# Performance work log

Measured on AMD Instinct MI355X. Metric: run time of the kernel, lower is better.

Reference implementation:

```python
import jax, jax.numpy as jnp
import numpy as np

H = 256
V_IN = 32000
V_OUT = 32000
T = 2048


def setup_inputs() -> dict:
    key = jax.random.key(0)
    ks = jax.random.split(key, 16)
    s = 1.0 / np.sqrt(H)
    inp = {
        "src": jax.random.randint(ks[0], (T, 1), 0, V_IN, dtype=jnp.int64 if jax.config.jax_enable_x64 else jnp.int32),
        "trg": jax.random.randint(ks[1], (T, 1), 0, V_OUT, dtype=jnp.int64 if jax.config.jax_enable_x64 else jnp.int32),
        "enc_emb": jax.random.normal(ks[2], (V_IN, H), jnp.float32),
        "enc_W_ih": jax.random.uniform(ks[3], (3 * H, H), jnp.float32, -s, s),
        "enc_W_hh": jax.random.uniform(ks[4], (3 * H, H), jnp.float32, -s, s),
        "enc_b_ih": jax.random.uniform(ks[5], (3 * H,), jnp.float32, -s, s),
        "enc_b_hh": jax.random.uniform(ks[6], (3 * H,), jnp.float32, -s, s),
        "dec_emb": jax.random.normal(ks[7], (V_OUT, H), jnp.float32),
        "dec_W_ih": jax.random.uniform(ks[8], (3 * H, H), jnp.float32, -s, s),
        "dec_W_hh": jax.random.uniform(ks[9], (3 * H, H), jnp.float32, -s, s),
        "dec_b_ih": jax.random.uniform(ks[10], (3 * H,), jnp.float32, -s, s),
        "dec_b_hh": jax.random.uniform(ks[11], (3 * H,), jnp.float32, -s, s),
        "out_W": jax.random.uniform(ks[12], (V_OUT, H), jnp.float32, -s, s),
        "out_b": jax.random.uniform(ks[13], (V_OUT,), jnp.float32, -s, s),
    }
    return inp


def _gru_step(x, h, W_ih, W_hh, b_ih, b_hh):
    # PyTorch GRU cell math. x,h: [H]
    gi = W_ih @ x + b_ih          # [3H]
    gh = W_hh @ h + b_hh          # [3H]
    i_r, i_z, i_n = jnp.split(gi, 3)
    h_r, h_z, h_n = jnp.split(gh, 3)
    r = jax.nn.sigmoid(i_r + h_r)
    z = jax.nn.sigmoid(i_z + h_z)
    n = jnp.tanh(i_n + r * h_n)
    return (1.0 - z) * n + z * h


def reference(src, trg, enc_emb, enc_W_ih, enc_W_hh, enc_b_ih, enc_b_hh,
              dec_emb, dec_W_ih, dec_W_hh, dec_b_ih, dec_b_hh, out_W, out_b):
    src_t = src[:, 0]  # [T], batch forced to 1 by .view(1,1,-1)
    trg_t = trg[:, 0]  # [T]
    h0 = jnp.zeros((H,), enc_emb.dtype)

    def step(h, toks):
        s_tok, t_tok = toks
        # encoder step
        h = _gru_step(enc_emb[s_tok], h, enc_W_ih, enc_W_hh, enc_b_ih, enc_b_hh)
        # decoder step (relu on embedding per source)
        x_d = jax.nn.relu(dec_emb[t_tok])
        h = _gru_step(x_d, h, dec_W_ih, dec_W_hh, dec_b_ih, dec_b_hh)
        logits = out_W @ h + out_b          # [V_OUT]
        return h, jax.nn.log_softmax(logits)

    _, outs = jax.lax.scan(step, h0, (src_t, trg_t))
    return outs[:, None, :]  # [T, 1, V_OUT]
```

## Files before the change

### kernel.cpp

```cpp
#include <hip/hip_runtime.h>
#include <hip/hip_bf16.h>

#define T_STEPS 2048
#define HDIM 256
#define VOUT 32000

typedef short short8 __attribute__((ext_vector_type(8)));
typedef float f32x4 __attribute__((ext_vector_type(4)));

#if defined(__has_builtin)
#if __has_builtin(__builtin_amdgcn_sdot4)
#define HAVE_SDOT4 1
#endif
#if __has_builtin(__builtin_amdgcn_mov_dpp)
#define HAVE_DPP 1
#endif
#endif

__device__ __forceinline__ int dot4i8(int a, int b, int c) {
#ifdef HAVE_SDOT4
    return __builtin_amdgcn_sdot4(a, b, c, false);
#else
#pragma unroll
    for (int k = 0; k < 4; ++k) {
        int av = (a << (24 - 8 * k)) >> 24;
        int bv = (b << (24 - 8 * k)) >> 24;
        c += av * bv;
    }
    return c;
#endif
}

__device__ __forceinline__ int pairsum(int x) {
#ifdef HAVE_DPP
    return x + __builtin_amdgcn_mov_dpp(x, 0xB1, 0xF, 0xF, true);
#else
    return x + __shfl_xor(x, 1);
#endif
}

__device__ __forceinline__ float fast_sigmoid(float x) {
    return 1.0f / (1.0f + __expf(-x));
}
__device__ __forceinline__ float fast_tanh(float x) {
    float ax = fabsf(x);
    float e = __expf(-2.0f * ax);
    float t = 1.0f - 2.0f * e / (1.0f + e);
    return copysignf(t, x);
}

__global__ void k_quant(const float* __restrict__ W, int* __restrict__ wq,
                        float* __restrict__ sc) {
    int row = blockIdx.x;
    int t = threadIdx.x;
    float4 w = ((const float4*)(W + (size_t)row * HDIM))[t];
    float m = fmaxf(fmaxf(fabsf(w.x), fabsf(w.y)), fmaxf(fabsf(w.z), fabsf(w.w)));
#pragma unroll
    for (int off = 32; off; off >>= 1) m = fmaxf(m, __shfl_xor(m, off));
    float inv = (m > 0.0f) ? 127.0f / m : 0.0f;
    float scale = (m > 0.0f) ? m * (1.0f / 127.0f) : 0.0f;
    int q0 = __float2int_rn(w.x * inv); q0 = max(-127, min(127, q0));
    int q1 = __float2int_rn(w.y * inv); q1 = max(-127, min(127, q1));
    int q2 = __float2int_rn(w.z * inv); q2 = max(-127, min(127, q2));
    int q3 = __float2int_rn(w.w * inv); q3 = max(-127, min(127, q3));
    int packed = (q0 & 255) | ((q1 & 255) << 8) | ((q2 & 255) << 16) | ((q3 & 255) << 24);
    wq[row * 64 + t] = packed;
    if (t == 0) sc[row] = scale;
}

__global__ __launch_bounds__(256) void k_cvt(const float* __restrict__ in,
                                             unsigned short* __restrict__ out, int n4) {
    int i = blockIdx.x * 256 + threadIdx.x;
    if (i < n4) {
        float4 v = ((const float4*)in)[i];
        unsigned int u[4] = {__float_as_uint(v.x), __float_as_uint(v.y),
                             __float_as_uint(v.z), __float_as_uint(v.w)};
        ushort4 o;
        o.x = (unsigned short)((u[0] + 0x7FFFu + ((u[0] >> 16) & 1)) >> 16);
        o.y = (unsigned short)((u[1] + 0x7FFFu + ((u[1] >> 16) & 1)) >> 16);
        o.z = (unsigned short)((u[2] + 0x7FFFu + ((u[2] >> 16) & 1)) >> 16);
        o.w = (unsigned short)((u[3] + 0x7FFFu + ((u[3] >> 16) & 1)) >> 16);
        ((ushort4*)out)[i] = o;
    }
}

__global__ __launch_bounds__(256) void k_gi(const int* __restrict__ toks,
                                            const float* __restrict__ emb,
                                            const float* __restrict__ W,
                                            const float* __restrict__ b,
                                            float* __restrict__ gi, int do_relu) {
    __shared__ float4 xs[64];
    int t = blockIdx.x;
    int tid = threadIdx.x;
    int tok = toks[t];
    if (tid < 64) {
        float4 x = ((const float4*)(emb + (size_t)tok * HDIM))[tid];
        if (do_relu) {
            x.x = fmaxf(x.x, 0.0f); x.y = fmaxf(x.y, 0.0f);
            x.z = fmaxf(x.z, 0.0f); x.w = fmaxf(x.w, 0.0f);
        }
        xs[tid] = x;
    }
    __syncthreads();
#pragma unroll
    for (int g = 0; g < 3; ++g) {
        int row = tid + g * 256;
        const float4* wr = (const float4*)(W + (size_t)row * HDIM);
        float acc = b[row];
#pragma unroll 16
        for (int k = 0; k < 64; ++k) {
            float4 w = wr[k];
            float4 x = xs[k];
            acc += w.x * x.x + w.y * x.y + w.z * x.z + w.w * x.w;
        }
        gi[(size_t)t * 768 + row] = acc;
    }
}

__global__ __launch_bounds__(512, 2) void k_gru(
    const int* __restrict__ wq_e, const float* __restrict__ sc_e,
    const float* __restrict__ bhh_e, const float* __restrict__ gi_e,
    const int* __restrict__ wq_d, const float* __restrict__ sc_d,
    const float* __restrict__ bhh_d, const float* __restrict__ gi_d,
    unsigned short* __restrict__ h_bf) {
    __shared__ __align__(16) int HQ[2][64];

    const int tid = threadIdx.x;
    const int rg = tid >> 1;
    const int c  = tid & 1;

    int we[3][32], wd[3][32];
    float se[3], sd[3], be[3], bd[3];
#pragma unroll
    for (int j = 0; j < 3; ++j) {
        const int row = rg + j * 256;
        const int4* pe = (const int4*)(wq_e + (row * 64 + c * 32));
        const int4* pd = (const int4*)(wq_d + (row * 64 + c * 32));
#pragma unroll
        for (int i = 0; i < 8; ++i) {
            int4 a = pe[i];
            we[j][4 * i + 0] = a.x; we[j][4 * i + 1] = a.y;
            we[j][4 * i + 2] = a.z; we[j][4 * i + 3] = a.w;
            int4 bq = pd[i];
            wd[j][4 * i + 0] = bq.x; wd[j][4 * i + 1] = bq.y;
            wd[j][4 * i + 2] = bq.z; wd[j][4 * i + 3] = bq.w;
        }
        se[j] = sc_e[row] * (1.0f / 127.0f);
        sd[j] = sc_d[row] * (1.0f / 127.0f);
        be[j] = bhh_e[row];
        bd[j] = bhh_d[row];
    }

    float h = 0.0f;
    if (tid < 64) HQ[0][tid] = 0;
    __syncthreads();

    const float* ge = gi_e + rg;
    const float* gd = gi_d + rg;
    unsigned short* hop = h_bf + rg;
    int cur = 0;

    for (int t = 0; t < T_STEPS; ++t) {
        {
            float g0 = ge[0], g1 = ge[256], g2 = ge[512]; ge += 768;
            const int4* hq4 = ((const int4*)HQ[cur]) + c * 8;
            int p0 = 0, p1 = 0, p2 = 0;
#pragma unroll
            for (int i = 0; i < 8; ++i) {
                int4 v = hq4[i];
                p0 = dot4i8(we[0][4 * i + 0], v.x, p0);
                p1 = dot4i8(we[1][4 * i + 0], v.x, p1);
                p2 = dot4i8(we[2][4 * i + 0], v.x, p2);
                p0 = dot4i8(we[0][4 * i + 1], v.y, p0);
                p1 = dot4i8(we[1][4 * i + 1], v.y, p1);
                p2 = dot4i8(we[2][4 * i + 1], v.y, p2);
                p0 = dot4i8(we[0][4 * i + 2], v.z, p0);
                p1 = dot4i8(we[1][4 * i + 2], v.z, p1);
                p2 = dot4i8(we[2][4 * i + 2], v.z, p2);
                p0 = dot4i8(we[0][4 * i + 3], v.w, p0);
                p1 = dot4i8(we[1][4 * i + 3], v.w, p1);
                p2 = dot4i8(we[2][4 * i + 3], v.w, p2);
            }
            int f0 = pairsum(p0), f1 = pairsum(p1), f2 = pairsum(p2);
            float r = fast_sigmoid(g0 + se[0] * (float)f0 + be[0]);
            float z = fast_sigmoid(g1 + se[1] * (float)f1 + be[1]);
            float n = fast_tanh(g2 + r * (se[2] * (float)f2 + be[2]));
            h = (1.0f - z) * n + z * h;
            if (c == 0)
                ((signed char*)HQ[cur ^ 1])[rg] = (signed char)__float2int_rn(h * 127.0f);
        }
        __syncthreads();
        cur ^= 1;

        {
            float g0 = gd[0], g1 = gd[256], g2 = gd[512]; gd += 768;
            const int4* hq4 = ((const int4*)HQ[cur]) + c * 8;
            int p0 = 0, p1 = 0, p2 = 0;
#pragma unroll
            for (int i = 0; i < 8; ++i) {
                int4 v = hq4[i];
                p0 = dot4i8(wd[0][4 * i + 0], v.x, p0);
                p1 = dot4i8(wd[1][4 * i + 0], v.x, p1);
                p2 = dot4i8(wd[2][4 * i + 0], v.x, p2);
                p0 = dot4i8(wd[0][4 * i + 1], v.y, p0);
                p1 = dot4i8(wd[1][4 * i + 1], v.y, p1);
                p2 = dot4i8(wd[2][4 * i + 1], v.y, p2);
                p0 = dot4i8(wd[0][4 * i + 2], v.z, p0);
                p1 = dot4i8(wd[1][4 * i + 2], v.z, p1);
                p2 = dot4i8(wd[2][4 * i + 2], v.z, p2);
                p0 = dot4i8(wd[0][4 * i + 3], v.w, p0);
                p1 = dot4i8(wd[1][4 * i + 3], v.w, p1);
                p2 = dot4i8(wd[2][4 * i + 3], v.w, p2);
            }
            int f0 = pairsum(p0), f1 = pairsum(p1), f2 = pairsum(p2);
            float r = fast_sigmoid(g0 + sd[0] * (float)f0 + bd[0]);
            float z = fast_sigmoid(g1 + sd[1] * (float)f1 + bd[1]);
            float n = fast_tanh(g2 + r * (sd[2] * (float)f2 + bd[2]));
            h = (1.0f - z) * n + z * h;
            if (c == 0) {
                ((signed char*)HQ[cur ^ 1])[rg] = (signed char)__float2int_rn(h * 127.0f);
                unsigned int u = __float_as_uint(h);
                *hop = (unsigned short)((u + 0x7FFFu + ((u >> 16) & 1)) >> 16);
            }
            hop += 256;
        }
        __syncthreads();
        cur ^= 1;
    }
}

__global__ __launch_bounds__(256) void k_logits(const unsigned short* __restrict__ hb,
                                                const unsigned short* __restrict__ wb,
                                                const float* __restrict__ out_b,
                                                float* __restrict__ out) {
    const int vb = blockIdx.x * 64;
    const int tb = blockIdx.y * 64;
    const int w = threadIdx.x >> 6;
    const int l = threadIdx.x & 63;
    const int m = l & 15;
    const int q = l >> 4;

    const unsigned short* aptr = hb + (size_t)(tb + w * 16 + m) * HDIM + q * 8;
    const unsigned short* bptr = wb + (size_t)(vb + m) * HDIM + q * 8;

    short8 af[8];
#pragma unroll
    for (int kt = 0; kt < 8; ++kt) af[kt] = *(const short8*)(aptr + kt * 32);

    f32x4 acc[4];
#pragma unroll
    for (int nt = 0; nt < 4; ++nt)
#pragma unroll
        for (int r = 0; r < 4; ++r) acc[nt][r] = 0.0f;

#pragma unroll
    for (int nt = 0; nt < 4; ++nt) {
        const unsigned short* bp = bptr + (size_t)nt * 16 * HDIM;
#pragma unroll
        for (int kt = 0; kt < 8; ++kt) {
            short8 bf = *(const short8*)(bp + kt * 32);
            acc[nt] = __builtin_amdgcn_mfma_f32_16x16x32_bf16(af[kt], bf, acc[nt], 0, 0, 0);
        }
    }
#pragma unroll
    for (int nt = 0; nt < 4; ++nt) {
        float bias = out_b[vb + nt * 16 + m];
#pragma unroll
        for (int r = 0; r < 4; ++r) {
            out[(size_t)(tb + w * 16 + q * 4 + r) * VOUT + vb + nt * 16 + m] =
                acc[nt][r] + bias;
        }
    }
}

__global__ __launch_bounds__(256) void k_lse(const float* __restrict__ out,
                                             float* __restrict__ lse) {
    const int t = blockIdx.x;
    const int tid = threadIdx.x;
    const float* rowp = out + (size_t)t * VOUT;
    float m = -3.0e38f, l = 0.0f;
    for (int v = tid; v < VOUT; v += 256) {
        float x = rowp[v];
        float M = fmaxf(m, x);
        l = l * __expf(m - M) + __expf(x - M);
        m = M;
    }
#pragma unroll
    for (int off = 32; off; off >>= 1) {
        float m2 = __shfl_xor(m, off);
        float l2 = __shfl_xor(l, off);
        float M = fmaxf(m, m2);
        l = l * __expf(m - M) + l2 * __expf(m2 - M);
        m = M;
    }
    __shared__ float sm[4], sl[4];
    int lane = tid & 63, wv = tid >> 6;
    if (lane == 0) { sm[wv] = m; sl[wv] = l; }
    __syncthreads();
    if (tid == 0) {
        float M = fmaxf(fmaxf(sm[0], sm[1]), fmaxf(sm[2], sm[3]));
        float L = sl[0] * __expf(sm[0] - M) + sl[1] * __expf(sm[1] - M) +
                  sl[2] * __expf(sm[2] - M) + sl[3] * __expf(sm[3] - M);
        lse[t] = M + __logf(L);
    }
}

__global__ __launch_bounds__(256) void k_sub(float* __restrict__ out,
                                             const float* __restrict__ lse) {
    const int t = blockIdx.y;
    const int v4 = blockIdx.x * 256 + threadIdx.x;
    if (v4 < VOUT / 4) {
        float s = lse[t];
        float4* p = (float4*)(out + (size_t)t * VOUT) + v4;
        float4 o = *p;
        o.x -= s; o.y -= s; o.z -= s; o.w -= s;
        *p = o;
    }
}

extern "C" void kernel_launch(void* const* d_in, const int* in_sizes, int n_in,
                              void* d_out, int out_size, void* d_ws, size_t ws_size,
                              hipStream_t stream) {
    (void)in_sizes; (void)n_in; (void)out_size; (void)ws_size;
    const int*   src      = (const int*)d_in[0];
    const int*   trg      = (const int*)d_in[1];
    const float* enc_emb  = (const float*)d_in[2];
    const float* enc_W_ih = (const float*)d_in[3];
    const float* enc_W_hh = (const float*)d_in[4];
    const float* enc_b_ih = (const float*)d_in[5];
    const float* enc_b_hh = (const float*)d_in[6];
    const float* dec_emb  = (const float*)d_in[7];
    const float* dec_W_ih = (const float*)d_in[8];
    const float* dec_W_hh = (const float*)d_in[9];
    const float* dec_b_ih = (const float*)d_in[10];
    const float* dec_b_hh = (const float*)d_in[11];
    const float* out_W    = (const float*)d_in[12];
    const float* out_b    = (const float*)d_in[13];
    float* out = (float*)d_out;

    char* ws = (char*)d_ws;
    float* gi_e  = (float*)ws; ws += (size_t)T_STEPS * 768 * 4;
    float* gi_d  = (float*)ws; ws += (size_t)T_STEPS * 768 * 4;
    float* lse   = (float*)ws; ws += (size_t)T_STEPS * 4;
    float* sc_e  = (float*)ws; ws += 768 * 4;
    float* sc_d  = (float*)ws; ws += 768 * 4;
    int*   wq_e  = (int*)ws;   ws += 768 * 64 * 4;
    int*   wq_d  = (int*)ws;   ws += 768 * 64 * 4;
    unsigned short* h_bf = (unsigned short*)ws; ws += (size_t)T_STEPS * HDIM * 2;
    unsigned short* w_bf = (unsigned short*)ws; ws += (size_t)VOUT * HDIM * 2;

    k_quant<<<768, 64, 0, stream>>>(enc_W_hh, wq_e, sc_e);
    k_quant<<<768, 64, 0, stream>>>(dec_W_hh, wq_d, sc_d);
    k_cvt<<<(VOUT * HDIM / 4 + 255) / 256, 256, 0, stream>>>(out_W, w_bf, VOUT * HDIM / 4);
    k_gi<<<T_STEPS, 256, 0, stream>>>(src, enc_emb, enc_W_ih, enc_b_ih, gi_e, 0);
    k_gi<<<T_STEPS, 256, 0, stream>>>(trg, dec_emb, dec_W_ih, dec_b_ih, gi_d, 1);
    k_gru<<<1, 512, 0, stream>>>(wq_e, sc_e, enc_b_hh, gi_e,
                                 wq_d, sc_d, dec_b_hh, gi_d, h_bf);
    k_logits<<<dim3(VOUT / 64, T_STEPS / 64), 256, 0, stream>>>(h_bf, w_bf, out_b, out);
    k_lse<<<T_STEPS, 256, 0, stream>>>(out, lse);
    k_sub<<<dim3(32, T_STEPS), 256, 0, stream>>>(out, lse);
}
```

Measured before the change: 4.171 ms.

## Fuse log-sum-exp with subtraction, prefetch gate inputs, use rcp in GRU activations

Merges the lse and subtract kernels into one per-row kernel, so the separate launch and the lse buffer round trip go away. The row is read a second time, likely from cache. In the single-block GRU recurrence, the encoder and decoder input-gate values are now prefetched one phase early to hide global load latency on the serial critical path. The ping-pong index is replaced with two fixed shared buffers, and sigmoid and tanh now use hardware reciprocal instead of full division, which slightly changes numerics.

```diff
diff --git a/kernel.cpp b/kernel.cpp
--- a/kernel.cpp
+++ b/kernel.cpp
@@ -14,6 +14,9 @@
 #endif
 #if __has_builtin(__builtin_amdgcn_mov_dpp)
 #define HAVE_DPP 1
+#endif
+#if __has_builtin(__builtin_amdgcn_rcpf)
+#define HAVE_RCP 1
 #endif
 #endif
 
@@ -39,13 +42,21 @@
 #endif
 }
 
+__device__ __forceinline__ float fast_rcp(float x) {
+#ifdef HAVE_RCP
+    return __builtin_amdgcn_rcpf(x);
+#else
+    return 1.0f / x;
+#endif
+}
+
 __device__ __forceinline__ float fast_sigmoid(float x) {
-    return 1.0f / (1.0f + __expf(-x));
+    return fast_rcp(1.0f + __expf(-x));
 }
 __device__ __forceinline__ float fast_tanh(float x) {
     float ax = fabsf(x);
     float e = __expf(-2.0f * ax);
-    float t = 1.0f - 2.0f * e / (1.0f + e);
+    float t = 1.0f - 2.0f * e * fast_rcp(1.0f + e);
     return copysignf(t, x);
 }
 
@@ -123,7 +134,8 @@
     const int* __restrict__ wq_d, const float* __restrict__ sc_d,
     const float* __restrict__ bhh_d, const float* __restrict__ gi_d,
     unsigned short* __restrict__ h_bf) {
-    __shared__ __align__(16) int HQ[2][64];
+    __shared__ __align__(16) int HQA[64];
+    __shared__ __align__(16) int HQB[64];
 
     const int tid = threadIdx.x;
     const int rg = tid >> 1;
@@ -152,18 +164,21 @@
     }
 
     float h = 0.0f;
-    if (tid < 64) HQ[0][tid] = 0;
+    if (tid < 64) HQA[tid] = 0;
     __syncthreads();
 
     const float* ge = gi_e + rg;
     const float* gd = gi_d + rg;
     unsigned short* hop = h_bf + rg;
-    int cur = 0;
+
+    float eg0 = ge[0], eg1 = ge[256], eg2 = ge[512];
 
     for (int t = 0; t < T_STEPS; ++t) {
+        float dg0 = gd[0], dg1 = gd[256], dg2 = gd[512];
+        gd += 768;
+
         {
-            float g0 = ge[0], g1 = ge[256], g2 = ge[512]; ge += 768;
-            const int4* hq4 = ((const int4*)HQ[cur]) + c * 8;
+            const int4* hq4 = ((const int4*)HQA) + c * 8;
             int p0 = 0, p1 = 0, p2 = 0;
 #pragma unroll
             for (int i = 0; i < 8; ++i) {
@@ -182,19 +197,23 @@
                 p2 = dot4i8(we[2][4 * i + 3], v.w, p2);
             }
             int f0 = pairsum(p0), f1 = pairsum(p1), f2 = pairsum(p2);
-            float r = fast_sigmoid(g0 + se[0] * (float)f0 + be[0]);
-            float z = fast_sigmoid(g1 + se[1] * (float)f1 + be[1]);
-            float n = fast_tanh(g2 + r * (se[2] * (float)f2 + be[2]));
+            float r = fast_sigmoid(eg0 + se[0] * (float)f0 + be[0]);
+            float z = fast_sigmoid(eg1 + se[1] * (float)f1 + be[1]);
+            float n = fast_tanh(eg2 + r * (se[2] * (float)f2 + be[2]));
             h = (1.0f - z) * n + z * h;
             if (c == 0)
-                ((signed char*)HQ[cur ^ 1])[rg] = (signed char)__float2int_rn(h * 127.0f);
+                ((signed char*)HQB)[rg] = (signed char)__float2int_rn(h * 127.0f);
         }
         __syncthreads();
-        cur ^= 1;
 
         {
-            float g0 = gd[0], g1 = gd[256], g2 = gd[512]; gd += 768;
-            const int4* hq4 = ((const int4*)HQ[cur]) + c * 8;
+            const float* gen = (t < T_STEPS - 1) ? (ge + 768) : (gi_e + rg);
+            eg0 = gen[0]; eg1 = gen[256]; eg2 = gen[512];
+            ge = gen;
+        }
+
+        {
+            const int4* hq4 = ((const int4*)HQB) + c * 8;
             int p0 = 0, p1 = 0, p2 = 0;
 #pragma unroll
             for (int i = 0; i < 8; ++i) {
@@ -213,19 +232,18 @@
                 p2 = dot4i8(wd[2][4 * i + 3], v.w, p2);
             }
             int f0 = pairsum(p0), f1 = pairsum(p1), f2 = pairsum(p2);
-            float r = fast_sigmoid(g0 + sd[0] * (float)f0 + bd[0]);
-            float z = fast_sigmoid(g1 + sd[1] * (float)f1 + bd[1]);
-            float n = fast_tanh(g2 + r * (sd[2] * (float)f2 + bd[2]));
+            float r = fast_sigmoid(dg0 + sd[0] * (float)f0 + bd[0]);
+            float z = fast_sigmoid(dg1 + sd[1] * (float)f1 + bd[1]);
+            float n = fast_tanh(dg2 + r * (sd[2] * (float)f2 + bd[2]));
             h = (1.0f - z) * n + z * h;
             if (c == 0) {
-                ((signed char*)HQ[cur ^ 1])[rg] = (signed char)__float2int_rn(h * 127.0f);
+                ((signed char*)HQA)[rg] = (signed char)__float2int_rn(h * 127.0f);
                 unsigned int u = __float_as_uint(h);
                 *hop = (unsigned short)((u + 0x7FFFu + ((u >> 16) & 1)) >> 16);
             }
             hop += 256;
         }
         __syncthreads();
-        cur ^= 1;
     }
 }
 
@@ -273,11 +291,10 @@
     }
 }
 
-__global__ __launch_bounds__(256) void k_lse(const float* __restrict__ out,
-                                             float* __restrict__ lse) {
+__global__ __launch_bounds__(256) void k_lsesub(float* __restrict__ out) {
     const int t = blockIdx.x;
     const int tid = threadIdx.x;
-    const float* rowp = out + (size_t)t * VOUT;
+    float* rowp = out + (size_t)t * VOUT;
     float m = -3.0e38f, l = 0.0f;
     for (int v = tid; v < VOUT; v += 256) {
         float x = rowp[v];
@@ -294,6 +311,7 @@
         m = M;
     }
     __shared__ float sm[4], sl[4];
+    __shared__ float s_lse;
     int lane = tid & 63, wv = tid >> 6;
     if (lane == 0) { sm[wv] = m; sl[wv] = l; }
     __syncthreads();
@@ -301,20 +319,15 @@
         float M = fmaxf(fmaxf(sm[0], sm[1]), fmaxf(sm[2], sm[3]));
         float L = sl[0] * __expf(sm[0] - M) + sl[1] * __expf(sm[1] - M) +
                   sl[2] * __expf(sm[2] - M) + sl[3] * __expf(sm[3] - M);
-        lse[t] = M + __logf(L);
-    }
-}
-
-__global__ __launch_bounds__(256) void k_sub(float* __restrict__ out,
-                                             const float* __restrict__ lse) {
-    const int t = blockIdx.y;
-    const int v4 = blockIdx.x * 256 + threadIdx.x;
-    if (v4 < VOUT / 4) {
-        float s = lse[t];
-        float4* p = (float4*)(out + (size_t)t * VOUT) + v4;
-        float4 o = *p;
+        s_lse = M + __logf(L);
+    }
+    __syncthreads();
+    float s = s_lse;
+    float4* p4 = (float4*)rowp;
+    for (int i = tid; i < VOUT / 4; i += 256) {
+        float4 o = p4[i];
         o.x -= s; o.y -= s; o.z -= s; o.w -= s;
-        *p = o;
+        p4[i] = o;
     }
 }
 
@@ -341,7 +354,6 @@
     char* ws = (char*)d_ws;
     float* gi_e  = (float*)ws; ws += (size_t)T_STEPS * 768 * 4;
     float* gi_d  = (float*)ws; ws += (size_t)T_STEPS * 768 * 4;
-    float* lse   = (float*)ws; ws += (size_t)T_STEPS * 4;
     float* sc_e  = (float*)ws; ws += 768 * 4;
     float* sc_d  = (float*)ws; ws += 768 * 4;
     int*   wq_e  = (int*)ws;   ws += 768 * 64 * 4;
@@ -357,6 +369,5 @@
     k_gru<<<1, 512, 0, stream>>>(wq_e, sc_e, enc_b_hh, gi_e,
                                  wq_d, sc_d, dec_b_hh, gi_d, h_bf);
     k_logits<<<dim3(VOUT / 64, T_STEPS / 64), 256, 0, stream>>>(h_bf, w_bf, out_b, out);
-    k_lse<<<T_STEPS, 256, 0, stream>>>(out, lse);
-    k_sub<<<dim3(32, T_STEPS), 256, 0, stream>>>(out, lse);
-}
+    k_lsesub<<<T_STEPS, 256, 0, stream>>>(out);
+}
```

Result: faster. 3.783 ms (-9.3%).
